# Performance work log

Hardware: AMD Instinct MI355X
Metric: run time of the kernel (lower is better)

Reference implementation:

```python
import jax, jax.numpy as jnp
import numpy as np
from jax import lax

B, C, IC, H, W = 4, 64, 32, 64, 64


def _conv(x, w, b, stride, pad):
    y = lax.conv_general_dilated(
        x, w, (stride, stride), [(pad, pad), (pad, pad)],
        dimension_numbers=('NCHW', 'OIHW', 'NCHW'))
    return y + b[None, :, None, None]


def setup_inputs() -> dict:
    key = jax.random.key(0)
    ks = jax.random.split(key, 15)
    s = 0.05
    inp = {
        'x': jax.random.normal(ks[0], (B, C, H, W), jnp.float32),
        # GEunit convs (3x3)
        'd1_w': jax.random.normal(ks[1], (C, C, 3, 3), jnp.float32) * s,
        'd1_b': jax.random.normal(ks[2], (C,), jnp.float32) * s,
        'd2_w': jax.random.normal(ks[3], (C, C, 3, 3), jnp.float32) * s,
        'd2_b': jax.random.normal(ks[4], (C,), jnp.float32) * s,
        'd3_w': jax.random.normal(ks[5], (C, C, 3, 3), jnp.float32) * s,
        'd3_b': jax.random.normal(ks[6], (C,), jnp.float32) * s,
        # 1x1 projections
        'g_w': jax.random.normal(ks[7], (IC, C, 1, 1), jnp.float32) * s,
        'g_b': jax.random.normal(ks[8], (IC,), jnp.float32) * s,
        'th_w': jax.random.normal(ks[9], (IC, C, 1, 1), jnp.float32) * s,
        'th_b': jax.random.normal(ks[10], (IC,), jnp.float32) * s,
        'ph_w': jax.random.normal(ks[11], (IC, C, 1, 1), jnp.float32) * s,
        'ph_b': jax.random.normal(ks[12], (IC,), jnp.float32) * s,
        # output projection (zero-init in original; random here for nontrivial baseline)
        'w_w': jax.random.normal(ks[13], (C, IC, 1, 1), jnp.float32) * s,
        'w_b': jax.random.normal(ks[14], (C,), jnp.float32) * s,
    }
    return inp


def _forward(x, d1_w, d1_b, d2_w, d2_b, d3_w, d3_b,
             g_w, g_b, th_w, th_b, ph_w, ph_b, w_w, w_b):
    lrelu = lambda v: jnp.where(v >= 0, v, 0.2 * v)
    y = lrelu(_conv(x, d1_w, d1_b, 2, 1))
    y = lrelu(_conv(y, d2_w, d2_b, 2, 1))
    y = _conv(y, d3_w, d3_b, 2, 1)
    y = jax.image.resize(y, (x.shape[0], x.shape[1], x.shape[2], x.shape[3]),
                         method='bilinear')  # align_corners=False equivalent
    am = jax.nn.sigmoid(y) * x  # attention_map, [B,C,H,W]

    b, c, h, w = am.shape
    n = h * w
    g_x = _conv(am, g_w, g_b, 1, 0).reshape(b, IC, n)      # [B,IC,N]
    theta = _conv(am, th_w, th_b, 1, 0).reshape(b, IC, n)  # [B,IC,N]
    phi = _conv(am, ph_w, ph_b, 1, 0).reshape(b, IC, n)    # [B,IC,N]

    # f[b,i,j] = theta[:, i] . phi[:, j];  softmax over dim=1 (the i axis)
    f = jnp.einsum('bci,bcj->bij', theta, phi)             # [B,N,N]
    f_div_C = jax.nn.softmax(f, axis=1)
    y2 = jnp.einsum('bij,bjc->bic', f_div_C, g_x.transpose(0, 2, 1))  # [B,N,IC]
    y2 = y2.transpose(0, 2, 1).reshape(b, IC, h, w)

    W_y = _conv(y2, w_w, w_b, 1, 0)
    z = W_y + am
    return z * x


def reference(x, d1_w, d1_b, d2_w, d2_b, d3_w, d3_b,
              g_w, g_b, th_w, th_b, ph_w, ph_b, w_w, w_b):
    return _forward(x, d1_w, d1_b, d2_w, d2_b, d3_w, d3_b,
                    g_w, g_b, th_w, th_b, ph_w, ph_b, w_w, w_b)
```

## Files before the change

### kernel.cpp

```cpp
#include <hip/hip_runtime.h>

#define B_ 4
#define C_ 64
#define IC_ 32
#define N_ 4096
#define LOG2E 1.44269504088896341f

typedef __attribute__((ext_vector_type(8))) short short8;
typedef __attribute__((ext_vector_type(4))) float floatx4;

__device__ __forceinline__ unsigned short f2bf(float f) {
  unsigned u = __float_as_uint(f);
  u += 0x7FFFu + ((u >> 16) & 1u);
  return (unsigned short)(u >> 16);
}
__device__ __forceinline__ float bf2f(unsigned short h) {
  return __uint_as_float(((unsigned)h) << 16);
}

__global__ void __launch_bounds__(256) pack_xw_k(
    const float* __restrict__ x, unsigned short* __restrict__ xclp,
    const float* __restrict__ d1_w, const float* __restrict__ d2_w, const float* __restrict__ d3_w,
    const float* __restrict__ th_w, const float* __restrict__ ph_w, const float* __restrict__ g_w,
    const float* __restrict__ th_b, const float* __restrict__ ph_b, const float* __restrict__ g_b,
    unsigned short* __restrict__ wpk, unsigned short* __restrict__ wproj, float* __restrict__ bproj,
    unsigned short* __restrict__ y1clp, unsigned short* __restrict__ y2clp)
{
  __shared__ float s[64][65];
  const int t = threadIdx.x;
  if (blockIdx.x < 256) {
    const int b = blockIdx.x >> 6, h = blockIdx.x & 63;
    for (int idx = t; idx < 4096; idx += 256) {
      int c = idx >> 6, w = idx & 63;
      s[c][w] = x[((size_t)(b * 64 + c)) * 4096 + h * 64 + w];
    }
    __syncthreads();
    for (int idx = t; idx < 4096; idx += 256) {
      int w = idx >> 6, c = idx & 63;
      xclp[(((size_t)b * 66 + h + 1) * 66 + (w + 1)) * 64 + c] = f2bf(s[c][w]);
    }
  } else {
    const int tid = (blockIdx.x - 256) * 256 + t;
    for (int idx = tid; idx < 3 * 36864; idx += 16 * 256) {
      int cv = idx / 36864, r = idx % 36864;
      int tap = r / 4096, r2 = r % 4096;
      int oc = r2 >> 6, ic = r2 & 63;
      const float* src = (cv == 0) ? d1_w : (cv == 1) ? d2_w : d3_w;
      wpk[(size_t)cv * 36864 + tap * 4096 + oc * 64 + ic] = f2bf(src[oc * 576 + ic * 9 + tap]);
    }
    for (int idx = tid; idx < 6144; idx += 16 * 256) {
      int m = idx >> 6, ic = idx & 63;
      float v = (m < 32) ? LOG2E * th_w[m * 64 + ic]
              : (m < 64) ? ph_w[(m - 32) * 64 + ic]
                         : g_w[(m - 64) * 64 + ic];
      wproj[m * 64 + ic] = f2bf(v);
    }
    for (int m = tid; m < 96; m += 16 * 256) {
      bproj[m] = (m < 32) ? LOG2E * th_b[m] : (m < 64) ? ph_b[m - 32] : g_b[m - 64];
    }
    const uint4 z4 = {0u, 0u, 0u, 0u};
    for (int idx = tid; idx < 4 * 4356; idx += 4096) {
      int r = idx % 4356, h = r / 66, w = r % 66;
      if (h == 0 || h == 65 || w == 0 || w == 65) {
        uint4* d = reinterpret_cast<uint4*>(xclp + (size_t)idx * 64);
#pragma unroll
        for (int q = 0; q < 8; ++q) d[q] = z4;
      }
    }
    for (int idx = tid; idx < 4 * 1156; idx += 4096) {
      int r = idx % 1156, h = r / 34, w = r % 34;
      if (h == 0 || h == 33 || w == 0 || w == 33) {
        uint4* d = reinterpret_cast<uint4*>(y1clp + (size_t)idx * 64);
#pragma unroll
        for (int q = 0; q < 8; ++q) d[q] = z4;
      }
    }
    for (int idx = tid; idx < 4 * 324; idx += 4096) {
      int r = idx % 324, h = r / 18, w = r % 18;
      if (h == 0 || h == 17 || w == 0 || w == 17) {
        uint4* d = reinterpret_cast<uint4*>(y2clp + (size_t)idx * 64);
#pragma unroll
        for (int q = 0; q < 8; ++q) d[q] = z4;
      }
    }
  }
}

template<int IN_PW, int OUT_H>
__global__ void __launch_bounds__(64) convmf_k(
    const unsigned short* __restrict__ xin, const unsigned short* __restrict__ wp,
    const float* __restrict__ bias, unsigned short* __restrict__ obf)
{
  constexpr int NTILES = OUT_H * OUT_H / 16;
  const int lane = threadIdx.x;
  const int n15 = lane & 15, quad = lane >> 4;
  int bx = blockIdx.x;
  const int opair = bx & 1; bx >>= 1;
  const int otile = bx % NTILES;
  const int b = bx / NTILES;
  const int o = otile * 16 + n15;
  const int oh = o / OUT_H, ow = o % OUT_H;
  const unsigned short* xb = xin + (size_t)b * IN_PW * IN_PW * 64;
  floatx4 acc0 = {0.f, 0.f, 0.f, 0.f}, acc1 = {0.f, 0.f, 0.f, 0.f};
#pragma unroll
  for (int tap = 0; tap < 9; ++tap) {
    const int kh = tap / 3, kw = tap % 3;
    const unsigned short* xpix = xb + ((size_t)(oh * 2 + kh) * IN_PW + (ow * 2 + kw)) * 64;
#pragma unroll
    for (int ks = 0; ks < 2; ++ks) {
      short8 bf = *reinterpret_cast<const short8*>(xpix + ks * 32 + quad * 8);
      short8 af0 = *reinterpret_cast<const short8*>(
          wp + ((size_t)tap * 64 + (opair * 2 + 0) * 16 + n15) * 64 + ks * 32 + quad * 8);
      short8 af1 = *reinterpret_cast<const short8*>(
          wp + ((size_t)tap * 64 + (opair * 2 + 1) * 16 + n15) * 64 + ks * 32 + quad * 8);
      acc0 = __builtin_amdgcn_mfma_f32_16x16x32_bf16(af0, bf, acc0, 0, 0, 0);
      acc1 = __builtin_amdgcn_mfma_f32_16x16x32_bf16(af1, bf, acc1, 0, 0, 0);
    }
  }
  constexpr int OPW = OUT_H + 2;
  const float4 bv0 = *reinterpret_cast<const float4*>(bias + (opair * 2 + 0) * 16 + quad * 4);
  const float4 bv1 = *reinterpret_cast<const float4*>(bias + (opair * 2 + 1) * 16 + quad * 4);
  float v0[4] = {acc0[0] + bv0.x, acc0[1] + bv0.y, acc0[2] + bv0.z, acc0[3] + bv0.w};
  float v1[4] = {acc1[0] + bv1.x, acc1[1] + bv1.y, acc1[2] + bv1.z, acc1[3] + bv1.w};
  unsigned short pk0[4], pk1[4];
#pragma unroll
  for (int r = 0; r < 4; ++r) {
    v0[r] = (v0[r] >= 0.f) ? v0[r] : 0.2f * v0[r];
    v1[r] = (v1[r] >= 0.f) ? v1[r] : 0.2f * v1[r];
    pk0[r] = f2bf(v0[r]); pk1[r] = f2bf(v1[r]);
  }
  unsigned short* orow = obf + (((size_t)b * OPW + oh + 1) * OPW + (ow + 1)) * 64;
  *reinterpret_cast<uint2*>(orow + (opair * 2 + 0) * 16 + quad * 4) = *reinterpret_cast<uint2*>(pk0);
  *reinterpret_cast<uint2*>(orow + (opair * 2 + 1) * 16 + quad * 4) = *reinterpret_cast<uint2*>(pk1);
}

__global__ void __launch_bounds__(256) upsproj_k(
    const unsigned short* __restrict__ y2clp, const unsigned short* __restrict__ wp3,
    const float* __restrict__ b3, const float* __restrict__ x,
    const unsigned short* __restrict__ wproj, const float* __restrict__ bproj,
    unsigned short* __restrict__ am_cl, unsigned short* __restrict__ thph,
    unsigned short* __restrict__ g16)
{
  const int b = blockIdx.x >> 6, oh = blockIdx.x & 63;
  const int t = threadIdx.x;
  __shared__ float s0[8 * 68], s1[8 * 68];
  __shared__ unsigned short s_am[64][72];
  float sh = (oh + 0.5f) * 0.125f - 0.5f;
  float fh = floorf(sh); float ah = sh - fh; int h0 = (int)fh;
  int h0c = min(7, max(0, h0)), h1c = min(7, max(0, h0 + 1));
  {
    const int wave = t >> 6, lane = t & 63;
    const int n15 = lane & 15, quad = lane >> 4;
    const int hrow = (n15 < 8) ? h0c : h1c;
    const int ow8 = n15 & 7;
    const unsigned short* xb2 = y2clp + (size_t)b * 18 * 18 * 64;
    floatx4 acc = {0.f, 0.f, 0.f, 0.f};
#pragma unroll
    for (int tap = 0; tap < 9; ++tap) {
      const int kh = tap / 3, kw = tap % 3;
      const unsigned short* xpix = xb2 + ((size_t)(hrow * 2 + kh) * 18 + (ow8 * 2 + kw)) * 64;
#pragma unroll
      for (int ks = 0; ks < 2; ++ks) {
        short8 af = *reinterpret_cast<const short8*>(
            wp3 + ((size_t)tap * 64 + wave * 16 + n15) * 64 + ks * 32 + quad * 8);
        short8 bf = *reinterpret_cast<const short8*>(xpix + ks * 32 + quad * 8);
        acc = __builtin_amdgcn_mfma_f32_16x16x32_bf16(af, bf, acc, 0, 0, 0);
      }
    }
    const float4 bv = *reinterpret_cast<const float4*>(b3 + wave * 16 + quad * 4);
    float4 st = {acc[0] + bv.x, acc[1] + bv.y, acc[2] + bv.z, acc[3] + bv.w};
    float* dst = (n15 < 8) ? s0 : s1;
    *reinterpret_cast<float4*>(&dst[(size_t)ow8 * 68 + wave * 16 + quad * 4]) = st;
  }
  __syncthreads();
  {
    const int ow = t >> 2, cq = t & 3;
    float sw = (ow + 0.5f) * 0.125f - 0.5f;
    float fw = floorf(sw); float aw = sw - fw; int w0 = (int)fw;
    int w0c = min(7, max(0, w0)), w1c = min(7, max(0, w0 + 1));
    const int n = oh * 64 + ow;
    const float* xb = x + (size_t)b * 64 * 4096 + n;
    unsigned short* ap = am_cl + ((size_t)b * N_ + n) * 64 + cq * 16;
#pragma unroll
    for (int u = 0; u < 4; ++u) {
      int c0 = cq * 16 + u * 4;
      float4 a00 = *reinterpret_cast<const float4*>(&s0[w0c * 68 + c0]);
      float4 a01 = *reinterpret_cast<const float4*>(&s0[w1c * 68 + c0]);
      float4 a10 = *reinterpret_cast<const float4*>(&s1[w0c * 68 + c0]);
      float4 a11 = *reinterpret_cast<const float4*>(&s1[w1c * 68 + c0]);
      float i0[4] = {a00.x * (1.f - aw) + a01.x * aw, a00.y * (1.f - aw) + a01.y * aw,
                     a00.z * (1.f - aw) + a01.z * aw, a00.w * (1.f - aw) + a01.w * aw};
      float i1[4] = {a10.x * (1.f - aw) + a11.x * aw, a10.y * (1.f - aw) + a11.y * aw,
                     a10.z * (1.f - aw) + a11.z * aw, a10.w * (1.f - aw) + a11.w * aw};
      unsigned short pk[4];
#pragma unroll
      for (int vi = 0; vi < 4; ++vi) {
        float vv = i0[vi] * (1.f - ah) + i1[vi] * ah;
        float xv = xb[(size_t)(c0 + vi) * 4096];
        float sig = 1.f / (1.f + __expf(-vv));
        pk[vi] = f2bf(sig * xv);
      }
      uint2 pkt = *reinterpret_cast<uint2*>(pk);
      *reinterpret_cast<uint2*>(ap + u * 4) = pkt;
      *reinterpret_cast<uint2*>(&s_am[ow][c0]) = pkt;
    }
  }
  __syncthreads();
  const int wave = t >> 6, lane = t & 63;
  const int n15 = lane & 15, quad = lane >> 4;
  const int n = oh * 64 + wave * 16 + n15;
  const unsigned short* srow = &s_am[wave * 16 + n15][0];
  const short8 bf0 = *reinterpret_cast<const short8*>(srow + quad * 8);
  const short8 bf1 = *reinterpret_cast<const short8*>(srow + 32 + quad * 8);
#pragma unroll
  for (int mt = 0; mt < 6; ++mt) {
    short8 a0 = *reinterpret_cast<const short8*>(wproj + ((size_t)mt * 16 + n15) * 64 + quad * 8);
    short8 a1 = *reinterpret_cast<const short8*>(wproj + ((size_t)mt * 16 + n15) * 64 + 32 + quad * 8);
    floatx4 acc = {0.f, 0.f, 0.f, 0.f};
    acc = __builtin_amdgcn_mfma_f32_16x16x32_bf16(a0, bf0, acc, 0, 0, 0);
    acc = __builtin_amdgcn_mfma_f32_16x16x32_bf16(a1, bf1, acc, 0, 0, 0);
    const float4 bv = *reinterpret_cast<const float4*>(bproj + mt * 16 + quad * 4);
    float v[4] = {acc[0] + bv.x, acc[1] + bv.y, acc[2] + bv.z, acc[3] + bv.w};
    if (mt < 4) {
      unsigned short pk[4];
#pragma unroll
      for (int r = 0; r < 4; ++r) pk[r] = f2bf(v[r]);
      *reinterpret_cast<uint2*>(thph + ((size_t)b * N_ + n) * 64 + mt * 16 + quad * 4) =
          *reinterpret_cast<uint2*>(pk);
    } else {
#pragma unroll
      for (int r = 0; r < 4; ++r)
        g16[((size_t)b * 32 + (mt - 4) * 16 + quad * 4 + r) * N_ + n] = f2bf(v[r]);
    }
  }
}

__global__ void __launch_bounds__(256) attn_stats_k(
    const unsigned short* __restrict__ thph, float* __restrict__ lpart)
{
  const int b  = blockIdx.y;
  const int iz = blockIdx.z;
  const int t = threadIdx.x, wave = t >> 6, lane = t & 63;
  const int n15 = lane & 15, quad = lane >> 4;
  const int jw = blockIdx.x * 512 + wave * 128;
  const unsigned short* base = thph + (size_t)b * N_ * 64;
  short8 bv[8];
#pragma unroll
  for (int v = 0; v < 8; ++v)
    bv[v] = *reinterpret_cast<const short8*>(base + (size_t)(jw + v * 16 + n15) * 64 + 32 + quad * 8);
  float ls[8];
#pragma unroll
  for (int v = 0; v < 8; ++v) ls[v] = 0.f;
  const unsigned short* ap = base + (size_t)(iz * 256 + n15) * 64 + quad * 8;
  short8 ac = *reinterpret_cast<const short8*>(ap);
  for (int st = 0; st < 16; ++st) {
    short8 an = *reinterpret_cast<const short8*>(ap + (size_t)((st < 15) ? st + 1 : st) * 1024);
#pragma unroll
    for (int v = 0; v < 8; ++v) {
      floatx4 z = {0.f, 0.f, 0.f, 0.f};
      z = __builtin_amdgcn_mfma_f32_16x16x32_bf16(ac, bv[v], z, 0, 0, 0);
      ls[v] += (__builtin_amdgcn_exp2f(z[0]) + __builtin_amdgcn_exp2f(z[1]))
             + (__builtin_amdgcn_exp2f(z[2]) + __builtin_amdgcn_exp2f(z[3]));
    }
    ac = an;
  }
#pragma unroll
  for (int v = 0; v < 8; ++v) {
    ls[v] += __shfl_xor(ls[v], 16);
    ls[v] += __shfl_xor(ls[v], 32);
  }
  if (quad == 0) {
#pragma unroll
    for (int v = 0; v < 8; ++v)
      lpart[((size_t)iz * B_ + b) * N_ + jw + v * 16 + n15] = ls[v];
  }
}

#define PHI_PITCH 40
#define G_PITCH   136
__global__ void __launch_bounds__(256, 2) attn_pv_k(
    const unsigned short* __restrict__ thph, const unsigned short* __restrict__ g16,
    const float* __restrict__ lpart, unsigned short* __restrict__ y2p)
{
  const int b  = blockIdx.y;
  const int jh = blockIdx.z;
  const int t = threadIdx.x, wave = t >> 6, lane = t & 63;
  const int n15 = lane & 15, quad = lane >> 4;
  const int iw0 = blockIdx.x * 256 + wave * 64;
  const unsigned short* base = thph + (size_t)b * N_ * 64;
  const unsigned short* gs   = g16  + (size_t)b * 32 * N_;
  __shared__ unsigned short phi_lds[2][128 * PHI_PITCH];
  __shared__ unsigned short g_lds[2][32 * G_PITCH];
  __shared__ float rl_lds[512];

  const int jbase = jh * 512;
  for (int jj = t; jj < 512; jj += 256) {
    float l = 0.f;
#pragma unroll
    for (int iz = 0; iz < 16; ++iz) l += lpart[((size_t)iz * B_ + b) * N_ + jbase + jj];
    rl_lds[jj] = 1.f / l;
  }

  short8 bth[4];
#pragma unroll
  for (int k = 0; k < 4; ++k)
    bth[k] = *reinterpret_cast<const short8*>(base + (size_t)(iw0 + k * 16 + n15) * 64 + quad * 8);
  floatx4 Y[4][2];
#pragma unroll
  for (int k = 0; k < 4; ++k) {
    Y[k][0] = floatx4{0.f, 0.f, 0.f, 0.f};
    Y[k][1] = floatx4{0.f, 0.f, 0.f, 0.f};
  }

  const int rphi = wave * 32 + (lane >> 2), cph = lane & 3;
  const int cg   = wave * 8  + (lane >> 4), chg = lane & 15;

  uint4 sp0, sp1, sg0, sg1;
  sp0 = *reinterpret_cast<const uint4*>(base + (size_t)(jbase + rphi) * 64 + 32 + cph * 8);
  sp1 = *reinterpret_cast<const uint4*>(base + (size_t)(jbase + rphi + 16) * 64 + 32 + cph * 8);
  sg0 = *reinterpret_cast<const uint4*>(gs + (size_t)cg * N_ + jbase + chg * 8);
  sg1 = *reinterpret_cast<const uint4*>(gs + (size_t)(cg + 4) * N_ + jbase + chg * 8);
  __syncthreads();

#define PV_WRITE_STAGE(BUF, CHN)                                                     \
  {                                                                                  \
    *reinterpret_cast<uint4*>(&phi_lds[BUF][rphi * PHI_PITCH + cph * 8]) = sp0;      \
    *reinterpret_cast<uint4*>(&phi_lds[BUF][(rphi + 16) * PHI_PITCH + cph * 8]) = sp1;\
    const int jloc = (CHN) * 128 + chg * 8;                                          \
    float4 r0 = *reinterpret_cast<const float4*>(&rl_lds[jloc]);                     \
    float4 r1 = *reinterpret_cast<const float4*>(&rl_lds[jloc + 4]);                 \
    union U8s { uint4 u4; unsigned short us[8]; } ua, ub, oa, ob_;                   \
    ua.u4 = sg0; ub.u4 = sg1;                                                        \
    oa.us[0] = f2bf(bf2f(ua.us[0]) * r0.x); oa.us[1] = f2bf(bf2f(ua.us[1]) * r0.y);  \
    oa.us[2] = f2bf(bf2f(ua.us[2]) * r0.z); oa.us[3] = f2bf(bf2f(ua.us[3]) * r0.w);  \
    oa.us[4] = f2bf(bf2f(ua.us[4]) * r1.x); oa.us[5] = f2bf(bf2f(ua.us[5]) * r1.y);  \
    oa.us[6] = f2bf(bf2f(ua.us[6]) * r1.z); oa.us[7] = f2bf(bf2f(ua.us[7]) * r1.w);  \
    ob_.us[0] = f2bf(bf2f(ub.us[0]) * r0.x); ob_.us[1] = f2bf(bf2f(ub.us[1]) * r0.y);\
    ob_.us[2] = f2bf(bf2f(ub.us[2]) * r0.z); ob_.us[3] = f2bf(bf2f(ub.us[3]) * r0.w);\
    ob_.us[4] = f2bf(bf2f(ub.us[4]) * r1.x); ob_.us[5] = f2bf(bf2f(ub.us[5]) * r1.y);\
    ob_.us[6] = f2bf(bf2f(ub.us[6]) * r1.z); ob_.us[7] = f2bf(bf2f(ub.us[7]) * r1.w);\
    *reinterpret_cast<uint4*>(&g_lds[BUF][cg * G_PITCH + chg * 8]) = oa.u4;          \
    *reinterpret_cast<uint4*>(&g_lds[BUF][(cg + 4) * G_PITCH + chg * 8]) = ob_.u4;   \
  }

  PV_WRITE_STAGE(0, 0)
  __syncthreads();

  int j0 = jbase;
  for (int ch = 0; ch < 4; ++ch, j0 += 128) {
    const int cur = ch & 1;
    if (ch < 3) {
      const int jn = j0 + 128;
      sp0 = *reinterpret_cast<const uint4*>(base + (size_t)(jn + rphi) * 64 + 32 + cph * 8);
      sp1 = *reinterpret_cast<const uint4*>(base + (size_t)(jn + rphi + 16) * 64 + 32 + cph * 8);
      sg0 = *reinterpret_cast<const uint4*>(gs + (size_t)cg * N_ + jn + chg * 8);
      sg1 = *reinterpret_cast<const uint4*>(gs + (size_t)(cg + 4) * N_ + jn + chg * 8);
    }
    const unsigned short* phb = &phi_lds[cur][0];
    const unsigned short* glb = &g_lds[cur][0];
#pragma unroll
    for (int sg = 0; sg < 4; ++sg) {
      unsigned pk[4][4];
#pragma unroll
      for (int jtl = 0; jtl < 2; ++jtl) {
        const int jt = sg * 2 + jtl;
        short8 aph = *reinterpret_cast<const short8*>(phb + (jt * 16 + n15) * PHI_PITCH + quad * 8);
        floatx4 z[4];
#pragma unroll
        for (int k = 0; k < 4; ++k) {
          floatx4 zz = {0.f, 0.f, 0.f, 0.f};
          z[k] = __builtin_amdgcn_mfma_f32_16x16x32_bf16(aph, bth[k], zz, 0, 0, 0);
        }
#pragma unroll
        for (int k = 0; k < 4; ++k) {
          float e0 = __builtin_amdgcn_exp2f(z[k][0]), e1 = __builtin_amdgcn_exp2f(z[k][1]);
          float e2 = __builtin_amdgcn_exp2f(z[k][2]), e3 = __builtin_amdgcn_exp2f(z[k][3]);
          pk[k][jtl * 2 + 0] = __builtin_amdgcn_perm(__float_as_uint(e1), __float_as_uint(e0), 0x07060302);
          pk[k][jtl * 2 + 1] = __builtin_amdgcn_perm(__float_as_uint(e3), __float_as_uint(e2), 0x07060302);
        }
      }
      union { unsigned u[4]; short8 v; } gb0, gb1;
      const unsigned short* gr0 = glb + n15 * G_PITCH + sg * 32 + quad * 4;
      const unsigned short* gr1 = glb + (16 + n15) * G_PITCH + sg * 32 + quad * 4;
      uint2 lo0 = *reinterpret_cast<const uint2*>(gr0);
      uint2 hi0 = *reinterpret_cast<const uint2*>(gr0 + 16);
      uint2 lo1 = *reinterpret_cast<const uint2*>(gr1);
      uint2 hi1 = *reinterpret_cast<const uint2*>(gr1 + 16);
      gb0.u[0] = lo0.x; gb0.u[1] = lo0.y; gb0.u[2] = hi0.x; gb0.u[3] = hi0.y;
      gb1.u[0] = lo1.x; gb1.u[1] = lo1.y; gb1.u[2] = hi1.x; gb1.u[3] = hi1.y;
#pragma unroll
      for (int k = 0; k < 4; ++k) {
        union { unsigned u[4]; short8 v; } pa;
        pa.u[0] = pk[k][0]; pa.u[1] = pk[k][1]; pa.u[2] = pk[k][2]; pa.u[3] = pk[k][3];
        Y[k][0] = __builtin_amdgcn_mfma_f32_16x16x32_bf16(pa.v, gb0.v, Y[k][0], 0, 0, 0);
        Y[k][1] = __builtin_amdgcn_mfma_f32_16x16x32_bf16(pa.v, gb1.v, Y[k][1], 0, 0, 0);
      }
    }
    if (ch < 3) {
      const int nb = cur ^ 1;
      PV_WRITE_STAGE(nb, ch + 1)
    }
    __syncthreads();
  }
#undef PV_WRITE_STAGE
  const size_t orow = ((size_t)jh * B_ + b) * 32;
#pragma unroll
  for (int k = 0; k < 4; ++k) {
    unsigned w0[2], w1[2];
    w0[0] = ((unsigned)f2bf(Y[k][0][1]) << 16) | f2bf(Y[k][0][0]);
    w0[1] = ((unsigned)f2bf(Y[k][0][3]) << 16) | f2bf(Y[k][0][2]);
    w1[0] = ((unsigned)f2bf(Y[k][1][1]) << 16) | f2bf(Y[k][1][0]);
    w1[1] = ((unsigned)f2bf(Y[k][1][3]) << 16) | f2bf(Y[k][1][2]);
    *reinterpret_cast<uint2*>(y2p + (orow + n15) * N_ + iw0 + k * 16 + quad * 4) =
        *reinterpret_cast<uint2*>(w0);
    *reinterpret_cast<uint2*>(y2p + (orow + 16 + n15) * N_ + iw0 + k * 16 + quad * 4) =
        *reinterpret_cast<uint2*>(w1);
  }
}

__global__ void __launch_bounds__(256) final_k(
    const unsigned short* __restrict__ y2p, const float* __restrict__ w_w,
    const float* __restrict__ w_b, const unsigned short* __restrict__ am_cl,
    const float* __restrict__ x, float* __restrict__ out)
{
  __shared__ float sred[32 * 128];
  const int t = threadIdx.x;
  const int xw = blockIdx.x;
  const int yh = blockIdx.y;
  const int b  = blockIdx.z;
  for (int idx = t; idx < 4096; idx += 256) {
    const int c = idx >> 7, nl = idx & 127;
    const int n = xw * 128 + nl;
    float sv = 0.f;
#pragma unroll
    for (int ph = 0; ph < 8; ++ph)
      sv += bf2f(y2p[(((size_t)ph * B_ + b) * 32 + c) * N_ + n]);
    sred[idx] = sv;
  }
  __syncthreads();
  const int nl = t & 127, sub = t >> 7;
  const int n = xw * 128 + nl;
  const int o0 = yh * 32 + sub * 16;
  float a[16];
#pragma unroll
  for (int u = 0; u < 16; ++u) a[u] = w_b[o0 + u];
  for (int c = 0; c < 32; ++c) {
    const float sv = sred[c * 128 + nl];
#pragma unroll
    for (int u = 0; u < 16; ++u) a[u] += w_w[(o0 + u) * 32 + c] * sv;
  }
  const unsigned short* amp = am_cl + ((size_t)b * N_ + n) * 64 + o0;
  const short8 am0 = *reinterpret_cast<const short8*>(amp);
  const short8 am1 = *reinterpret_cast<const short8*>(amp + 8);
#pragma unroll
  for (int u = 0; u < 16; ++u) {
    const size_t off = ((size_t)b * 64 + o0 + u) * N_ + n;
    const float amv = bf2f((unsigned short)((u < 8) ? am0[u] : am1[u - 8]));
    out[off] = (a[u] + amv) * x[off];
  }
}

extern "C" void kernel_launch(void* const* d_in, const int* in_sizes, int n_in,
                              void* d_out, int out_size, void* d_ws, size_t ws_size,
                              hipStream_t stream) {
  const float* x    = (const float*)d_in[0];
  const float* d1_w = (const float*)d_in[1];
  const float* d1_b = (const float*)d_in[2];
  const float* d2_w = (const float*)d_in[3];
  const float* d2_b = (const float*)d_in[4];
  const float* d3_w = (const float*)d_in[5];
  const float* d3_b = (const float*)d_in[6];
  const float* g_w  = (const float*)d_in[7];
  const float* g_b  = (const float*)d_in[8];
  const float* th_w = (const float*)d_in[9];
  const float* th_b = (const float*)d_in[10];
  const float* ph_w = (const float*)d_in[11];
  const float* ph_b = (const float*)d_in[12];
  const float* w_w  = (const float*)d_in[13];
  const float* w_b  = (const float*)d_in[14];
  float* out = (float*)d_out;

  char* p = (char*)d_ws;
  unsigned short* am_cl = (unsigned short*)p;  p += (size_t)B_ * N_ * 64 * 2;
  unsigned short* thph  = (unsigned short*)p;  p += (size_t)B_ * N_ * 64 * 2;
  unsigned short* g16   = (unsigned short*)p;  p += (size_t)B_ * 32 * N_ * 2;
  float* lpart          = (float*)p;           p += (size_t)16 * B_ * N_ * 4;
  unsigned short* y2p   = (unsigned short*)p;  p += (size_t)8 * B_ * 32 * N_ * 2;
  unsigned short* wpk   = (unsigned short*)p;  p += (size_t)3 * 36864 * 2;
  unsigned short* wproj = (unsigned short*)p;  p += (size_t)96 * 64 * 2;
  float* bproj          = (float*)p;           p += (size_t)96 * 4;
  unsigned short* xclp  = (unsigned short*)p;  p += (size_t)B_ * 66 * 66 * 64 * 2;
  unsigned short* y1clp = (unsigned short*)p;  p += (size_t)B_ * 34 * 34 * 64 * 2;
  unsigned short* y2clp = (unsigned short*)p;  p += (size_t)B_ * 18 * 18 * 64 * 2;

  pack_xw_k<<<272, 256, 0, stream>>>(x, xclp, d1_w, d2_w, d3_w, th_w, ph_w, g_w,
                                     th_b, ph_b, g_b, wpk, wproj, bproj, y1clp, y2clp);
  convmf_k<66, 32><<<512, 64, 0, stream>>>(xclp,  wpk,         d1_b, y1clp);
  convmf_k<34, 16><<<128, 64, 0, stream>>>(y1clp, wpk + 36864, d2_b, y2clp);
  upsproj_k<<<256, 256, 0, stream>>>(y2clp, wpk + 2 * 36864, d3_b, x, wproj, bproj,
                                     am_cl, thph, g16);
  attn_stats_k<<<dim3(8, 4, 16), 256, 0, stream>>>(thph, lpart);
  attn_pv_k<<<dim3(16, 4, 8), 256, 0, stream>>>(thph, g16, lpart, y2p);
  final_k<<<dim3(32, 2, 4), 256, 0, stream>>>(y2p, w_w, w_b, am_cl, x, out);
}
```

Measured before the change: 154.6 us.

## Split work finer across more blocks in pack, conv, upsample, stats and final kernels

Several kernels get smaller per-block work and larger grids. The pack kernel handles quarter rows, the conv kernels compute one 16-channel tile per block, upsproj covers 16 output columns per block, attn_stats covers 64 columns per wave, and final_k covers 64 pixels per block. The aim is to fill the MI355X's many CUs, since the small earlier grids left most of them idle. In exchange, upsproj now recomputes the 3x3 conv3 MFMA for every quarter-row block, which multiplies that redundant work by four. The smaller blocks also get less input reuse per block.

```diff
diff --git a/kernel.cpp b/kernel.cpp
--- a/kernel.cpp
+++ b/kernel.cpp
@@ -26,21 +26,22 @@
     unsigned short* __restrict__ wpk, unsigned short* __restrict__ wproj, float* __restrict__ bproj,
     unsigned short* __restrict__ y1clp, unsigned short* __restrict__ y2clp)
 {
-  __shared__ float s[64][65];
+  __shared__ float s[64][17];
   const int t = threadIdx.x;
-  if (blockIdx.x < 256) {
-    const int b = blockIdx.x >> 6, h = blockIdx.x & 63;
-    for (int idx = t; idx < 4096; idx += 256) {
-      int c = idx >> 6, w = idx & 63;
-      s[c][w] = x[((size_t)(b * 64 + c)) * 4096 + h * 64 + w];
+  if (blockIdx.x < 1024) {
+    const int va = blockIdx.x;
+    const int b = va >> 8, h = (va >> 2) & 63, q = va & 3;
+    for (int idx = t; idx < 1024; idx += 256) {
+      int c = idx >> 4, w = idx & 15;
+      s[c][w] = x[((size_t)(b * 64 + c)) * 4096 + h * 64 + q * 16 + w];
     }
     __syncthreads();
-    for (int idx = t; idx < 4096; idx += 256) {
+    for (int idx = t; idx < 1024; idx += 256) {
       int w = idx >> 6, c = idx & 63;
-      xclp[(((size_t)b * 66 + h + 1) * 66 + (w + 1)) * 64 + c] = f2bf(s[c][w]);
+      xclp[(((size_t)b * 66 + h + 1) * 66 + (q * 16 + w + 1)) * 64 + c] = f2bf(s[c][w]);
     }
   } else {
-    const int tid = (blockIdx.x - 256) * 256 + t;
+    const int tid = (blockIdx.x - 1024) * 256 + t;
     for (int idx = tid; idx < 3 * 36864; idx += 16 * 256) {
       int cv = idx / 36864, r = idx % 36864;
       int tap = r / 4096, r2 = r % 4096;
@@ -95,43 +96,36 @@
   const int lane = threadIdx.x;
   const int n15 = lane & 15, quad = lane >> 4;
   int bx = blockIdx.x;
-  const int opair = bx & 1; bx >>= 1;
+  const int octile = bx & 3; bx >>= 2;
   const int otile = bx % NTILES;
   const int b = bx / NTILES;
   const int o = otile * 16 + n15;
   const int oh = o / OUT_H, ow = o % OUT_H;
   const unsigned short* xb = xin + (size_t)b * IN_PW * IN_PW * 64;
-  floatx4 acc0 = {0.f, 0.f, 0.f, 0.f}, acc1 = {0.f, 0.f, 0.f, 0.f};
+  floatx4 acc = {0.f, 0.f, 0.f, 0.f};
 #pragma unroll
   for (int tap = 0; tap < 9; ++tap) {
     const int kh = tap / 3, kw = tap % 3;
     const unsigned short* xpix = xb + ((size_t)(oh * 2 + kh) * IN_PW + (ow * 2 + kw)) * 64;
 #pragma unroll
     for (int ks = 0; ks < 2; ++ks) {
+      short8 af = *reinterpret_cast<const short8*>(
+          wp + ((size_t)tap * 64 + octile * 16 + n15) * 64 + ks * 32 + quad * 8);
       short8 bf = *reinterpret_cast<const short8*>(xpix + ks * 32 + quad * 8);
-      short8 af0 = *reinterpret_cast<const short8*>(
-          wp + ((size_t)tap * 64 + (opair * 2 + 0) * 16 + n15) * 64 + ks * 32 + quad * 8);
-      short8 af1 = *reinterpret_cast<const short8*>(
-          wp + ((size_t)tap * 64 + (opair * 2 + 1) * 16 + n15) * 64 + ks * 32 + quad * 8);
-      acc0 = __builtin_amdgcn_mfma_f32_16x16x32_bf16(af0, bf, acc0, 0, 0, 0);
-      acc1 = __builtin_amdgcn_mfma_f32_16x16x32_bf16(af1, bf, acc1, 0, 0, 0);
-    }
-  }
+      acc = __builtin_amdgcn_mfma_f32_16x16x32_bf16(af, bf, acc, 0, 0, 0);
+    }
+  }
+  const float4 bv = *reinterpret_cast<const float4*>(bias + octile * 16 + quad * 4);
+  float v[4] = {acc[0] + bv.x, acc[1] + bv.y, acc[2] + bv.z, acc[3] + bv.w};
+#pragma unroll
+  for (int r = 0; r < 4; ++r) v[r] = (v[r] >= 0.f) ? v[r] : 0.2f * v[r];
   constexpr int OPW = OUT_H + 2;
-  const float4 bv0 = *reinterpret_cast<const float4*>(bias + (opair * 2 + 0) * 16 + quad * 4);
-  const float4 bv1 = *reinterpret_cast<const float4*>(bias + (opair * 2 + 1) * 16 + quad * 4);
-  float v0[4] = {acc0[0] + bv0.x, acc0[1] + bv0.y, acc0[2] + bv0.z, acc0[3] + bv0.w};
-  float v1[4] = {acc1[0] + bv1.x, acc1[1] + bv1.y, acc1[2] + bv1.z, acc1[3] + bv1.w};
-  unsigned short pk0[4], pk1[4];
-#pragma unroll
-  for (int r = 0; r < 4; ++r) {
-    v0[r] = (v0[r] >= 0.f) ? v0[r] : 0.2f * v0[r];
-    v1[r] = (v1[r] >= 0.f) ? v1[r] : 0.2f * v1[r];
-    pk0[r] = f2bf(v0[r]); pk1[r] = f2bf(v1[r]);
-  }
-  unsigned short* orow = obf + (((size_t)b * OPW + oh + 1) * OPW + (ow + 1)) * 64;
-  *reinterpret_cast<uint2*>(orow + (opair * 2 + 0) * 16 + quad * 4) = *reinterpret_cast<uint2*>(pk0);
-  *reinterpret_cast<uint2*>(orow + (opair * 2 + 1) * 16 + quad * 4) = *reinterpret_cast<uint2*>(pk1);
+  unsigned short pk[4];
+#pragma unroll
+  for (int r = 0; r < 4; ++r) pk[r] = f2bf(v[r]);
+  *reinterpret_cast<uint2*>(
+      obf + (((size_t)b * OPW + oh + 1) * OPW + (ow + 1)) * 64 + octile * 16 + quad * 4) =
+      *reinterpret_cast<uint2*>(pk);
 }
 
 __global__ void __launch_bounds__(256) upsproj_k(
@@ -141,16 +135,17 @@
     unsigned short* __restrict__ am_cl, unsigned short* __restrict__ thph,
     unsigned short* __restrict__ g16)
 {
-  const int b = blockIdx.x >> 6, oh = blockIdx.x & 63;
+  const int va = blockIdx.x;
+  const int b = va >> 8, oh = (va >> 2) & 63, owq = va & 3;
   const int t = threadIdx.x;
   __shared__ float s0[8 * 68], s1[8 * 68];
-  __shared__ unsigned short s_am[64][72];
+  __shared__ unsigned short s_am[16][72];
   float sh = (oh + 0.5f) * 0.125f - 0.5f;
   float fh = floorf(sh); float ah = sh - fh; int h0 = (int)fh;
   int h0c = min(7, max(0, h0)), h1c = min(7, max(0, h0 + 1));
+  const int wave = t >> 6, lane = t & 63;
+  const int n15 = lane & 15, quad = lane >> 4;
   {
-    const int wave = t >> 6, lane = t & 63;
-    const int n15 = lane & 15, quad = lane >> 4;
     const int hrow = (n15 < 8) ? h0c : h1c;
     const int ow8 = n15 & 7;
     const unsigned short* xb2 = y2clp + (size_t)b * 18 * 18 * 64;
@@ -174,63 +169,59 @@
   }
   __syncthreads();
   {
-    const int ow = t >> 2, cq = t & 3;
+    const int ow_l = t >> 4, cgrp = t & 15;
+    const int c0 = cgrp * 4;
+    const int ow = owq * 16 + ow_l;
     float sw = (ow + 0.5f) * 0.125f - 0.5f;
     float fw = floorf(sw); float aw = sw - fw; int w0 = (int)fw;
     int w0c = min(7, max(0, w0)), w1c = min(7, max(0, w0 + 1));
     const int n = oh * 64 + ow;
     const float* xb = x + (size_t)b * 64 * 4096 + n;
-    unsigned short* ap = am_cl + ((size_t)b * N_ + n) * 64 + cq * 16;
-#pragma unroll
-    for (int u = 0; u < 4; ++u) {
-      int c0 = cq * 16 + u * 4;
-      float4 a00 = *reinterpret_cast<const float4*>(&s0[w0c * 68 + c0]);
-      float4 a01 = *reinterpret_cast<const float4*>(&s0[w1c * 68 + c0]);
-      float4 a10 = *reinterpret_cast<const float4*>(&s1[w0c * 68 + c0]);
-      float4 a11 = *reinterpret_cast<const float4*>(&s1[w1c * 68 + c0]);
-      float i0[4] = {a00.x * (1.f - aw) + a01.x * aw, a00.y * (1.f - aw) + a01.y * aw,
-                     a00.z * (1.f - aw) + a01.z * aw, a00.w * (1.f - aw) + a01.w * aw};
-      float i1[4] = {a10.x * (1.f - aw) + a11.x * aw, a10.y * (1.f - aw) + a11.y * aw,
-                     a10.z * (1.f - aw) + a11.z * aw, a10.w * (1.f - aw) + a11.w * aw};
-      unsigned short pk[4];
-#pragma unroll
-      for (int vi = 0; vi < 4; ++vi) {
-        float vv = i0[vi] * (1.f - ah) + i1[vi] * ah;
-        float xv = xb[(size_t)(c0 + vi) * 4096];
-        float sig = 1.f / (1.f + __expf(-vv));
-        pk[vi] = f2bf(sig * xv);
-      }
-      uint2 pkt = *reinterpret_cast<uint2*>(pk);
-      *reinterpret_cast<uint2*>(ap + u * 4) = pkt;
-      *reinterpret_cast<uint2*>(&s_am[ow][c0]) = pkt;
-    }
+    float4 a00 = *reinterpret_cast<const float4*>(&s0[w0c * 68 + c0]);
+    float4 a01 = *reinterpret_cast<const float4*>(&s0[w1c * 68 + c0]);
+    float4 a10 = *reinterpret_cast<const float4*>(&s1[w0c * 68 + c0]);
+    float4 a11 = *reinterpret_cast<const float4*>(&s1[w1c * 68 + c0]);
+    float i0[4] = {a00.x * (1.f - aw) + a01.x * aw, a00.y * (1.f - aw) + a01.y * aw,
+                   a00.z * (1.f - aw) + a01.z * aw, a00.w * (1.f - aw) + a01.w * aw};
+    float i1[4] = {a10.x * (1.f - aw) + a11.x * aw, a10.y * (1.f - aw) + a11.y * aw,
+                   a10.z * (1.f - aw) + a11.z * aw, a10.w * (1.f - aw) + a11.w * aw};
+    unsigned short pk[4];
+#pragma unroll
+    for (int vi = 0; vi < 4; ++vi) {
+      float vv = i0[vi] * (1.f - ah) + i1[vi] * ah;
+      float xv = xb[(size_t)(c0 + vi) * 4096];
+      float sig = 1.f / (1.f + __expf(-vv));
+      pk[vi] = f2bf(sig * xv);
+    }
+    uint2 pkt = *reinterpret_cast<uint2*>(pk);
+    *reinterpret_cast<uint2*>(am_cl + ((size_t)b * N_ + n) * 64 + c0) = pkt;
+    *reinterpret_cast<uint2*>(&s_am[ow_l][c0]) = pkt;
   }
   __syncthreads();
-  const int wave = t >> 6, lane = t & 63;
-  const int n15 = lane & 15, quad = lane >> 4;
-  const int n = oh * 64 + wave * 16 + n15;
-  const unsigned short* srow = &s_am[wave * 16 + n15][0];
-  const short8 bf0 = *reinterpret_cast<const short8*>(srow + quad * 8);
-  const short8 bf1 = *reinterpret_cast<const short8*>(srow + 32 + quad * 8);
-#pragma unroll
-  for (int mt = 0; mt < 6; ++mt) {
-    short8 a0 = *reinterpret_cast<const short8*>(wproj + ((size_t)mt * 16 + n15) * 64 + quad * 8);
-    short8 a1 = *reinterpret_cast<const short8*>(wproj + ((size_t)mt * 16 + n15) * 64 + 32 + quad * 8);
-    floatx4 acc = {0.f, 0.f, 0.f, 0.f};
-    acc = __builtin_amdgcn_mfma_f32_16x16x32_bf16(a0, bf0, acc, 0, 0, 0);
-    acc = __builtin_amdgcn_mfma_f32_16x16x32_bf16(a1, bf1, acc, 0, 0, 0);
-    const float4 bv = *reinterpret_cast<const float4*>(bproj + mt * 16 + quad * 4);
-    float v[4] = {acc[0] + bv.x, acc[1] + bv.y, acc[2] + bv.z, acc[3] + bv.w};
-    if (mt < 4) {
-      unsigned short pk[4];
-#pragma unroll
-      for (int r = 0; r < 4; ++r) pk[r] = f2bf(v[r]);
-      *reinterpret_cast<uint2*>(thph + ((size_t)b * N_ + n) * 64 + mt * 16 + quad * 4) =
-          *reinterpret_cast<uint2*>(pk);
-    } else {
-#pragma unroll
-      for (int r = 0; r < 4; ++r)
-        g16[((size_t)b * 32 + (mt - 4) * 16 + quad * 4 + r) * N_ + n] = f2bf(v[r]);
+  {
+    const int n = oh * 64 + owq * 16 + n15;
+    const unsigned short* srow = &s_am[n15][0];
+    const short8 bf0 = *reinterpret_cast<const short8*>(srow + quad * 8);
+    const short8 bf1 = *reinterpret_cast<const short8*>(srow + 32 + quad * 8);
+    for (int mt = wave; mt < 6; mt += 4) {
+      short8 a0 = *reinterpret_cast<const short8*>(wproj + ((size_t)mt * 16 + n15) * 64 + quad * 8);
+      short8 a1 = *reinterpret_cast<const short8*>(wproj + ((size_t)mt * 16 + n15) * 64 + 32 + quad * 8);
+      floatx4 acc = {0.f, 0.f, 0.f, 0.f};
+      acc = __builtin_amdgcn_mfma_f32_16x16x32_bf16(a0, bf0, acc, 0, 0, 0);
+      acc = __builtin_amdgcn_mfma_f32_16x16x32_bf16(a1, bf1, acc, 0, 0, 0);
+      const float4 bv = *reinterpret_cast<const float4*>(bproj + mt * 16 + quad * 4);
+      float v[4] = {acc[0] + bv.x, acc[1] + bv.y, acc[2] + bv.z, acc[3] + bv.w};
+      if (mt < 4) {
+        unsigned short pk[4];
+#pragma unroll
+        for (int r = 0; r < 4; ++r) pk[r] = f2bf(v[r]);
+        *reinterpret_cast<uint2*>(thph + ((size_t)b * N_ + n) * 64 + mt * 16 + quad * 4) =
+            *reinterpret_cast<uint2*>(pk);
+      } else {
+#pragma unroll
+        for (int r = 0; r < 4; ++r)
+          g16[((size_t)b * 32 + (mt - 4) * 16 + quad * 4 + r) * N_ + n] = f2bf(v[r]);
+      }
     }
   }
 }
@@ -242,21 +233,19 @@
   const int iz = blockIdx.z;
   const int t = threadIdx.x, wave = t >> 6, lane = t & 63;
   const int n15 = lane & 15, quad = lane >> 4;
-  const int jw = blockIdx.x * 512 + wave * 128;
+  const int jw = blockIdx.x * 256 + wave * 64;
   const unsigned short* base = thph + (size_t)b * N_ * 64;
-  short8 bv[8];
-#pragma unroll
-  for (int v = 0; v < 8; ++v)
+  short8 bv[4];
+#pragma unroll
+  for (int v = 0; v < 4; ++v)
     bv[v] = *reinterpret_cast<const short8*>(base + (size_t)(jw + v * 16 + n15) * 64 + 32 + quad * 8);
-  float ls[8];
-#pragma unroll
-  for (int v = 0; v < 8; ++v) ls[v] = 0.f;
+  float ls[4] = {0.f, 0.f, 0.f, 0.f};
   const unsigned short* ap = base + (size_t)(iz * 256 + n15) * 64 + quad * 8;
   short8 ac = *reinterpret_cast<const short8*>(ap);
   for (int st = 0; st < 16; ++st) {
     short8 an = *reinterpret_cast<const short8*>(ap + (size_t)((st < 15) ? st + 1 : st) * 1024);
 #pragma unroll
-    for (int v = 0; v < 8; ++v) {
+    for (int v = 0; v < 4; ++v) {
       floatx4 z = {0.f, 0.f, 0.f, 0.f};
       z = __builtin_amdgcn_mfma_f32_16x16x32_bf16(ac, bv[v], z, 0, 0, 0);
       ls[v] += (__builtin_amdgcn_exp2f(z[0]) + __builtin_amdgcn_exp2f(z[1]))
@@ -265,13 +254,13 @@
     ac = an;
   }
 #pragma unroll
-  for (int v = 0; v < 8; ++v) {
+  for (int v = 0; v < 4; ++v) {
     ls[v] += __shfl_xor(ls[v], 16);
     ls[v] += __shfl_xor(ls[v], 32);
   }
   if (quad == 0) {
 #pragma unroll
-    for (int v = 0; v < 8; ++v)
+    for (int v = 0; v < 4; ++v)
       lpart[((size_t)iz * B_ + b) * N_ + jw + v * 16 + n15] = ls[v];
   }
 }
@@ -423,14 +412,14 @@
     const float* __restrict__ w_b, const unsigned short* __restrict__ am_cl,
     const float* __restrict__ x, float* __restrict__ out)
 {
-  __shared__ float sred[32 * 128];
+  __shared__ float sred[32 * 64];
   const int t = threadIdx.x;
   const int xw = blockIdx.x;
   const int yh = blockIdx.y;
   const int b  = blockIdx.z;
-  for (int idx = t; idx < 4096; idx += 256) {
-    const int c = idx >> 7, nl = idx & 127;
-    const int n = xw * 128 + nl;
+  for (int idx = t; idx < 2048; idx += 256) {
+    const int c = idx >> 6, nl = idx & 63;
+    const int n = xw * 64 + nl;
     float sv = 0.f;
 #pragma unroll
     for (int ph = 0; ph < 8; ++ph)
@@ -438,25 +427,22 @@
     sred[idx] = sv;
   }
   __syncthreads();
-  const int nl = t & 127, sub = t >> 7;
-  const int n = xw * 128 + nl;
-  const int o0 = yh * 32 + sub * 16;
-  float a[16];
-#pragma unroll
-  for (int u = 0; u < 16; ++u) a[u] = w_b[o0 + u];
+  const int nl = t & 63, sub = t >> 6;
+  const int n = xw * 64 + nl;
+  const int o0 = yh * 32 + sub * 8;
+  float a[8];
+#pragma unroll
+  for (int u = 0; u < 8; ++u) a[u] = w_b[o0 + u];
   for (int c = 0; c < 32; ++c) {
-    const float sv = sred[c * 128 + nl];
-#pragma unroll
-    for (int u = 0; u < 16; ++u) a[u] += w_w[(o0 + u) * 32 + c] * sv;
-  }
-  const unsigned short* amp = am_cl + ((size_t)b * N_ + n) * 64 + o0;
-  const short8 am0 = *reinterpret_cast<const short8*>(amp);
-  const short8 am1 = *reinterpret_cast<const short8*>(amp + 8);
-#pragma unroll
-  for (int u = 0; u < 16; ++u) {
+    const float sv = sred[c * 64 + nl];
+#pragma unroll
+    for (int u = 0; u < 8; ++u) a[u] += w_w[(o0 + u) * 32 + c] * sv;
+  }
+  const short8 am = *reinterpret_cast<const short8*>(am_cl + ((size_t)b * N_ + n) * 64 + o0);
+#pragma unroll
+  for (int u = 0; u < 8; ++u) {
     const size_t off = ((size_t)b * 64 + o0 + u) * N_ + n;
-    const float amv = bf2f((unsigned short)((u < 8) ? am0[u] : am1[u - 8]));
-    out[off] = (a[u] + amv) * x[off];
+    out[off] = (a[u] + bf2f((unsigned short)am[u])) * x[off];
   }
 }
 
@@ -493,13 +479,13 @@
   unsigned short* y1clp = (unsigned short*)p;  p += (size_t)B_ * 34 * 34 * 64 * 2;
   unsigned short* y2clp = (unsigned short*)p;  p += (size_t)B_ * 18 * 18 * 64 * 2;
 
-  pack_xw_k<<<272, 256, 0, stream>>>(x, xclp, d1_w, d2_w, d3_w, th_w, ph_w, g_w,
-                                     th_b, ph_b, g_b, wpk, wproj, bproj, y1clp, y2clp);
-  convmf_k<66, 32><<<512, 64, 0, stream>>>(xclp,  wpk,         d1_b, y1clp);
-  convmf_k<34, 16><<<128, 64, 0, stream>>>(y1clp, wpk + 36864, d2_b, y2clp);
-  upsproj_k<<<256, 256, 0, stream>>>(y2clp, wpk + 2 * 36864, d3_b, x, wproj, bproj,
-                                     am_cl, thph, g16);
-  attn_stats_k<<<dim3(8, 4, 16), 256, 0, stream>>>(thph, lpart);
+  pack_xw_k<<<1040, 256, 0, stream>>>(x, xclp, d1_w, d2_w, d3_w, th_w, ph_w, g_w,
+                                      th_b, ph_b, g_b, wpk, wproj, bproj, y1clp, y2clp);
+  convmf_k<66, 32><<<1024, 64, 0, stream>>>(xclp,  wpk,         d1_b, y1clp);
+  convmf_k<34, 16><<<256,  64, 0, stream>>>(y1clp, wpk + 36864, d2_b, y2clp);
+  upsproj_k<<<1024, 256, 0, stream>>>(y2clp, wpk + 2 * 36864, d3_b, x, wproj, bproj,
+                                      am_cl, thph, g16);
+  attn_stats_k<<<dim3(16, 4, 16), 256, 0, stream>>>(thph, lpart);
   attn_pv_k<<<dim3(16, 4, 8), 256, 0, stream>>>(thph, g16, lpart, y2p);
-  final_k<<<dim3(32, 2, 4), 256, 0, stream>>>(y2p, w_w, w_b, am_cl, x, out);
-}
+  final_k<<<dim3(64, 2, 4), 256, 0, stream>>>(y2p, w_w, w_b, am_cl, x, out);
+}
```

Result: slower. 171.8 us (+11.1%).
